# Kernel optimization log

Hardware: AMD Instinct MI355X
Metric: run time of the kernel (lower is better)

## Reference

```python
import jax, jax.numpy as jnp
import numpy as np

DIM = 512
PE_DIM = 64


def setup_inputs() -> dict:
    key = jax.random.key(0)
    k1, k2, k3, k4 = jax.random.split(key, 4)
    batch, heads, seqlen_kv = 64, 128, 4096
    return {
        "Q": jax.random.normal(k1, (batch, heads, DIM), dtype=jnp.float32),
        "Q_pe": jax.random.normal(k2, (batch, heads, PE_DIM), dtype=jnp.float32),
        "KV": jax.random.normal(k3, (batch, seqlen_kv, 1, DIM), dtype=jnp.float32),
        "K_pe": jax.random.normal(k4, (batch, seqlen_kv, 1, PE_DIM), dtype=jnp.float32),
    }


def reference(Q, Q_pe, KV, K_pe):
    # MLA decode attention with decoupled RoPE dim.
    # scores = Q @ KV^T + Q_pe @ K_pe^T, scaled by 1/sqrt(dim+pe_dim)
    # (kernel uses exp2 with log2(e)-folded scale; mathematically identical
    #  to standard softmax). Output = softmax(scores) @ KV.
    dim = Q.shape[-1]
    pe_dim = Q_pe.shape[-1]
    scale = 1.0 / np.sqrt(dim + pe_dim).astype(np.float32)
    kv = KV[:, :, 0, :]      # [b, s, dim]  (kv_head_num == 1)
    kpe = K_pe[:, :, 0, :]   # [b, s, pe_dim]
    scores = jnp.einsum('bhd,bsd->bhs', Q, kv)
    scores = scores + jnp.einsum('bhp,bsp->bhs', Q_pe, kpe)
    probs = jax.nn.softmax(scores * scale, axis=-1)  # [b, h, s]
    out = jnp.einsum('bhs,bsd->bhd', probs, kv)      # [b, h, dim]
    return out
```

## Files before the change

kernel.cpp:

```cpp
#include <hip/hip_runtime.h>

typedef _Float16 f16x8 __attribute__((ext_vector_type(8)));
typedef _Float16 f16x4 __attribute__((ext_vector_type(4)));
typedef float f32x4 __attribute__((ext_vector_type(4)));

#define B_SZ 64
#define H_SZ 128
#define S_SZ 4096
#define D_SZ 512
#define PE_SZ 64
#define NCHUNK 4
#define CHUNK 1024
#define NT 32
#define NTILES 32
#define CSCALE 0.06011229381f

#define STAGE_PITCH 516
#define KBUF_PITCH 584
#define VTB_PITCH 40
#define PB_PITCH 40
#define OB_PITCH 520

#define KBUF_OFF 66048
#define VTB_OFF 103424
#define PB_OFF 144384
#define SMEM_BYTES 154624

#define WSO_BYTES (64ull * 4 * 128 * 512 * 2)
#define WSM_OFF WSO_BYTES
#define WSL_OFF (WSO_BYTES + 64ull * 4 * 128 * 4)
#define WS_NEEDED (WSO_BYTES + 2ull * 64 * 4 * 128 * 4)

__device__ __forceinline__ void async_copy16(const float* g, float* l) {
  __builtin_amdgcn_global_load_lds(
      (const __attribute__((address_space(1))) void*)g,
      (__attribute__((address_space(3))) void*)l, 16, 0, 0);
}

__launch_bounds__(512, 2)
__global__ void mla_partial(const float* __restrict__ Q, const float* __restrict__ Qpe,
                            const float* __restrict__ KV, const float* __restrict__ Kpe,
                            _Float16* __restrict__ wsO, float* __restrict__ wsM,
                            float* __restrict__ wsL) {
  __shared__ __align__(16) char smem[SMEM_BYTES];
  float* stage   = (float*)smem;
  _Float16* kbuf = (_Float16*)(smem + KBUF_OFF);
  _Float16* vtb  = (_Float16*)(smem + VTB_OFF);
  _Float16* pb   = (_Float16*)(smem + PB_OFF);

  const int tid  = threadIdx.x;
  const int lane = tid & 63;
  const int w    = tid >> 6;
  const int quad = lane >> 4;
  const int l15  = lane & 15;

  const int b  = blockIdx.x >> 2;
  const int c  = blockIdx.x & 3;
  const int s0 = c * CHUNK;

  f16x8 qf[18];
  {
    const int h = w * 16 + l15;
    const float* qrow  = Q   + (size_t)(b * H_SZ + h) * D_SZ;
    const float* qprow = Qpe + (size_t)(b * H_SZ + h) * PE_SZ;
#pragma unroll
    for (int kk = 0; kk < 18; ++kk) {
      const float* src = (kk < 16) ? (qrow + kk * 32 + quad * 8)
                                   : (qprow + (kk - 16) * 32 + quad * 8);
      f32x4 a0 = *(const f32x4*)(src);
      f32x4 a1 = *(const f32x4*)(src + 4);
      f16x8 f;
      f[0] = (_Float16)a0[0]; f[1] = (_Float16)a0[1];
      f[2] = (_Float16)a0[2]; f[3] = (_Float16)a0[3];
      f[4] = (_Float16)a1[0]; f[5] = (_Float16)a1[1];
      f[6] = (_Float16)a1[2]; f[7] = (_Float16)a1[3];
      qf[kk] = f;
    }
  }

  f32x4 kpe_r;
  auto dma_tile = [&](int t, f32x4& kpe_out) {
    const int sg_base = b * S_SZ + s0 + t * NT;
#pragma unroll
    for (int rr = 0; rr < 4; ++rr) {
      const int row = w * 4 + rr;
      const float* gk = KV + (size_t)(sg_base + row) * D_SZ;
      float* l0 = stage + row * STAGE_PITCH;
      async_copy16(gk + lane * 4, l0 + lane * 4);
      async_copy16(gk + 256 + lane * 4, l0 + 256 + lane * 4);
    }
    kpe_out = *(const f32x4*)(Kpe + (size_t)sg_base * PE_SZ + tid * 4);
  };

  auto convert_tile = [&](f32x4 kpe_in) {
#pragma unroll
    for (int i = 0; i < 8; ++i) {
      int lin  = tid + 512 * i;
      int row  = lin >> 7;
      int col4 = lin & 127;
      f32x4 v = *(const f32x4*)(stage + row * STAGE_PITCH + col4 * 4);
      f16x4 h;
      h[0] = (_Float16)v[0]; h[1] = (_Float16)v[1];
      h[2] = (_Float16)v[2]; h[3] = (_Float16)v[3];
      *(f16x4*)(kbuf + row * KBUF_PITCH + col4 * 4) = h;
    }
    {
      int row  = tid >> 4;
      int col4 = tid & 15;
      f16x4 h;
      h[0] = (_Float16)kpe_in[0]; h[1] = (_Float16)kpe_in[1];
      h[2] = (_Float16)kpe_in[2]; h[3] = (_Float16)kpe_in[3];
      *(f16x4*)(kbuf + row * KBUF_PITCH + 512 + col4 * 4) = h;
    }
#pragma unroll
    for (int g = 0; g < 2; ++g) {
      int lin   = tid + 512 * g;
      int rg    = lin & 7;
      int cidx4 = lin >> 3;
      f32x4 v0 = *(const f32x4*)(stage + (rg * 4 + 0) * STAGE_PITCH + cidx4 * 4);
      f32x4 v1 = *(const f32x4*)(stage + (rg * 4 + 1) * STAGE_PITCH + cidx4 * 4);
      f32x4 v2 = *(const f32x4*)(stage + (rg * 4 + 2) * STAGE_PITCH + cidx4 * 4);
      f32x4 v3 = *(const f32x4*)(stage + (rg * 4 + 3) * STAGE_PITCH + cidx4 * 4);
#pragma unroll
      for (int u = 0; u < 4; ++u) {
        f16x4 h;
        h[0] = (_Float16)v0[u]; h[1] = (_Float16)v1[u];
        h[2] = (_Float16)v2[u]; h[3] = (_Float16)v3[u];
        *(f16x4*)(vtb + (cidx4 * 4 + u) * VTB_PITCH + rg * 4) = h;
      }
    }
  };

  f32x4 O[32];
#pragma unroll
  for (int i = 0; i < 32; ++i) O[i] = (f32x4){0.f, 0.f, 0.f, 0.f};
  f32x4 mr = (f32x4){-1e30f, -1e30f, -1e30f, -1e30f};
  f32x4 lr = (f32x4){0.f, 0.f, 0.f, 0.f};

  dma_tile(0, kpe_r);
  __syncthreads();
  convert_tile(kpe_r);
  __syncthreads();

  _Float16* pw = pb + w * 16 * PB_PITCH;

#pragma unroll 1
  for (int t = 0; t < NTILES; ++t) {
    f32x4 kpe_nxt;
    if (t < NTILES - 1) dma_tile(t + 1, kpe_nxt);

    f32x4 S0 = (f32x4){0.f, 0.f, 0.f, 0.f};
    f32x4 S1 = (f32x4){0.f, 0.f, 0.f, 0.f};
#pragma unroll
    for (int kk = 0; kk < 18; ++kk) {
      f16x8 b0 = *(const f16x8*)(kbuf + l15 * KBUF_PITCH + kk * 32 + quad * 8);
      f16x8 b1 = *(const f16x8*)(kbuf + (16 + l15) * KBUF_PITCH + kk * 32 + quad * 8);
      S0 = __builtin_amdgcn_mfma_f32_16x16x32_f16(qf[kk], b0, S0, 0, 0, 0);
      S1 = __builtin_amdgcn_mfma_f32_16x16x32_f16(qf[kk], b1, S1, 0, 0, 0);
    }

    f32x4 mx;
#pragma unroll
    for (int i = 0; i < 4; ++i) mx[i] = fmaxf(S0[i], S1[i]);
#pragma unroll
    for (int m = 1; m <= 8; m <<= 1) {
#pragma unroll
      for (int i = 0; i < 4; ++i) mx[i] = fmaxf(mx[i], __shfl_xor(mx[i], m, 64));
    }
    f32x4 mn, al, P0, P1, rs;
#pragma unroll
    for (int i = 0; i < 4; ++i) {
      mn[i] = fmaxf(mr[i], mx[i]);
      al[i] = exp2f((mr[i] - mn[i]) * CSCALE);
      P0[i] = exp2f((S0[i] - mn[i]) * CSCALE);
      P1[i] = exp2f((S1[i] - mn[i]) * CSCALE);
      rs[i] = P0[i] + P1[i];
    }
#pragma unroll
    for (int m = 1; m <= 8; m <<= 1) {
#pragma unroll
      for (int i = 0; i < 4; ++i) rs[i] += __shfl_xor(rs[i], m, 64);
    }
#pragma unroll
    for (int i = 0; i < 4; ++i) {
      lr[i] = lr[i] * al[i] + rs[i];
      mr[i] = mn[i];
    }

#pragma unroll
    for (int i = 0; i < 4; ++i) {
      pw[(quad * 4 + i) * PB_PITCH + l15]      = (_Float16)P0[i];
      pw[(quad * 4 + i) * PB_PITCH + 16 + l15] = (_Float16)P1[i];
    }
#pragma unroll
    for (int nt = 0; nt < 32; ++nt) O[nt] *= al;

    f16x8 pa = *(const f16x8*)(pw + l15 * PB_PITCH + quad * 8);
#pragma unroll
    for (int nt = 0; nt < 32; ++nt) {
      f16x8 bv = *(const f16x8*)(vtb + (nt * 16 + l15) * VTB_PITCH + quad * 8);
      O[nt] = __builtin_amdgcn_mfma_f32_16x16x32_f16(pa, bv, O[nt], 0, 0, 0);
    }

    __syncthreads();
    if (t < NTILES - 1) {
      convert_tile(kpe_nxt);
      __syncthreads();
    }
  }

  f32x4 inv;
#pragma unroll
  for (int i = 0; i < 4; ++i) inv[i] = 1.0f / lr[i];

  _Float16* ob = (_Float16*)smem;
#pragma unroll
  for (int nt = 0; nt < 32; ++nt) {
#pragma unroll
    for (int i = 0; i < 4; ++i) {
      ob[(w * 16 + quad * 4 + i) * OB_PITCH + nt * 16 + l15] =
          (_Float16)(O[nt][i] * inv[i]);
    }
  }
  __syncthreads();
  const size_t obase = (size_t)blockIdx.x * H_SZ * D_SZ;
#pragma unroll
  for (int j = 0; j < 16; ++j) {
    int idx = tid + 512 * j;
    int h   = idx >> 6;
    int d8  = (idx & 63) * 8;
    f16x8 v = *(const f16x8*)(ob + h * OB_PITCH + d8);
    *(f16x8*)(wsO + obase + h * D_SZ + d8) = v;
  }
  if (l15 == 0) {
    const int sbase = blockIdx.x * H_SZ + w * 16 + quad * 4;
#pragma unroll
    for (int i = 0; i < 4; ++i) {
      wsM[sbase + i] = mr[i];
      wsL[sbase + i] = lr[i];
    }
  }
}

__global__ void mla_combine(const _Float16* __restrict__ wsO, const float* __restrict__ wsM,
                            const float* __restrict__ wsL, float* __restrict__ out) {
  int tidg = blockIdx.x * 256 + threadIdx.x;
  int row  = tidg >> 6;
  int d8   = (tidg & 63) * 8;
  int b    = row >> 7;
  int h    = row & 127;

  float mv[4], lv[4];
#pragma unroll
  for (int c = 0; c < 4; ++c) {
    mv[c] = wsM[(b * 4 + c) * 128 + h];
    lv[c] = wsL[(b * 4 + c) * 128 + h];
  }
  float M = fmaxf(fmaxf(mv[0], mv[1]), fmaxf(mv[2], mv[3]));
  float wv[4], wsum = 0.f;
#pragma unroll
  for (int c = 0; c < 4; ++c) {
    wv[c] = lv[c] * exp2f((mv[c] - M) * CSCALE);
    wsum += wv[c];
  }
  float o[8] = {0.f, 0.f, 0.f, 0.f, 0.f, 0.f, 0.f, 0.f};
#pragma unroll
  for (int c = 0; c < 4; ++c) {
    f16x8 v = *(const f16x8*)(wsO + (size_t)((b * 4 + c) * 128 + h) * 512 + d8);
#pragma unroll
    for (int j = 0; j < 8; ++j) o[j] += wv[c] * (float)v[j];
  }
  float r = 1.0f / wsum;
  f32x4 r0 = (f32x4){o[0] * r, o[1] * r, o[2] * r, o[3] * r};
  f32x4 r1 = (f32x4){o[4] * r, o[5] * r, o[6] * r, o[7] * r};
  *(f32x4*)(out + (size_t)row * 512 + d8) = r0;
  *(f32x4*)(out + (size_t)row * 512 + d8 + 4) = r1;
}

extern "C" void kernel_launch(void* const* d_in, const int* in_sizes, int n_in,
                              void* d_out, int out_size, void* d_ws, size_t ws_size,
                              hipStream_t stream) {
  if (ws_size < WS_NEEDED) return;
  const float* Q   = (const float*)d_in[0];
  const float* Qpe = (const float*)d_in[1];
  const float* KV  = (const float*)d_in[2];
  const float* Kpe = (const float*)d_in[3];
  _Float16* wsO = (_Float16*)d_ws;
  float* wsM = (float*)((char*)d_ws + WSM_OFF);
  float* wsL = (float*)((char*)d_ws + WSL_OFF);

  mla_partial<<<dim3(B_SZ * NCHUNK), dim3(512), 0, stream>>>(Q, Qpe, KV, Kpe, wsO, wsM, wsL);
  mla_combine<<<dim3(2048), dim3(256), 0, stream>>>(wsO, wsM, wsL, (float*)d_out);
}
```

Measured before the change: 876.9 us.

## Transpose QK MFMA, defer softmax rescale, split PV across head-groups and D halves

The QK^T MFMA operands are swapped so each lane holds a full head row. This shrinks the row-max and row-sum reductions to two cross-quad shuffles. The running max is only raised when it grows past a threshold (lazy rescaling), and the O rescale is skipped when every alpha in the group is 1. The PV stage is re-partitioned so each wave computes 32 heads by 256 D columns, sharing its V-fragment loads across two P fragments. In exchange this adds a block barrier and LDS exchanges of P and alpha every tile, and deferred rescaling can let the probabilities reach 2^4 before fp16 conversion.

```diff
diff --git a/kernel.cpp b/kernel.cpp
--- a/kernel.cpp
+++ b/kernel.cpp
@@ -14,6 +14,7 @@
 #define NT 32
 #define NTILES 32
 #define CSCALE 0.06011229381f
+#define DEFER_LOG2 4.0f
 
 #define STAGE_PITCH 516
 #define KBUF_PITCH 584
@@ -24,7 +25,9 @@
 #define KBUF_OFF 66048
 #define VTB_OFF 103424
 #define PB_OFF 144384
-#define SMEM_BYTES 154624
+#define AL_OFF 154624
+#define LL_OFF 155136
+#define SMEM_BYTES 155648
 
 #define WSO_BYTES (64ull * 4 * 128 * 512 * 2)
 #define WSM_OFF WSO_BYTES
@@ -47,12 +50,16 @@
   _Float16* kbuf = (_Float16*)(smem + KBUF_OFF);
   _Float16* vtb  = (_Float16*)(smem + VTB_OFF);
   _Float16* pb   = (_Float16*)(smem + PB_OFF);
+  float* al_lds  = (float*)(smem + AL_OFF);
+  float* l_lds   = (float*)(smem + LL_OFF);
 
   const int tid  = threadIdx.x;
   const int lane = tid & 63;
   const int w    = tid >> 6;
   const int quad = lane >> 4;
   const int l15  = lane & 15;
+  const int hg   = w & 3;
+  const int dh   = w >> 2;
 
   const int b  = blockIdx.x >> 2;
   const int c  = blockIdx.x & 3;
@@ -134,8 +141,8 @@
   f32x4 O[32];
 #pragma unroll
   for (int i = 0; i < 32; ++i) O[i] = (f32x4){0.f, 0.f, 0.f, 0.f};
-  f32x4 mr = (f32x4){-1e30f, -1e30f, -1e30f, -1e30f};
-  f32x4 lr = (f32x4){0.f, 0.f, 0.f, 0.f};
+  float mr = -1e30f;
+  float lr = 0.f;
 
   dma_tile(0, kpe_r);
   __syncthreads();
@@ -151,55 +158,60 @@
 
     f32x4 S0 = (f32x4){0.f, 0.f, 0.f, 0.f};
     f32x4 S1 = (f32x4){0.f, 0.f, 0.f, 0.f};
+    const _Float16* kb0 = kbuf + l15 * KBUF_PITCH + quad * 8;
+    const _Float16* kb1 = kbuf + (16 + l15) * KBUF_PITCH + quad * 8;
 #pragma unroll
     for (int kk = 0; kk < 18; ++kk) {
-      f16x8 b0 = *(const f16x8*)(kbuf + l15 * KBUF_PITCH + kk * 32 + quad * 8);
-      f16x8 b1 = *(const f16x8*)(kbuf + (16 + l15) * KBUF_PITCH + kk * 32 + quad * 8);
-      S0 = __builtin_amdgcn_mfma_f32_16x16x32_f16(qf[kk], b0, S0, 0, 0, 0);
-      S1 = __builtin_amdgcn_mfma_f32_16x16x32_f16(qf[kk], b1, S1, 0, 0, 0);
-    }
-
-    f32x4 mx;
-#pragma unroll
-    for (int i = 0; i < 4; ++i) mx[i] = fmaxf(S0[i], S1[i]);
-#pragma unroll
-    for (int m = 1; m <= 8; m <<= 1) {
-#pragma unroll
-      for (int i = 0; i < 4; ++i) mx[i] = fmaxf(mx[i], __shfl_xor(mx[i], m, 64));
-    }
-    f32x4 mn, al, P0, P1, rs;
+      f16x8 b0 = *(const f16x8*)(kb0 + kk * 32);
+      f16x8 b1 = *(const f16x8*)(kb1 + kk * 32);
+      S0 = __builtin_amdgcn_mfma_f32_16x16x32_f16(b0, qf[kk], S0, 0, 0, 0);
+      S1 = __builtin_amdgcn_mfma_f32_16x16x32_f16(b1, qf[kk], S1, 0, 0, 0);
+    }
+
+    float mx = fmaxf(fmaxf(fmaxf(S0[0], S0[1]), fmaxf(S0[2], S0[3])),
+                     fmaxf(fmaxf(S1[0], S1[1]), fmaxf(S1[2], S1[3])));
+    mx = fmaxf(mx, __shfl_xor(mx, 16));
+    mx = fmaxf(mx, __shfl_xor(mx, 32));
+    const bool grow = (mx - mr) * CSCALE > DEFER_LOG2;
+    const float mn = grow ? mx : mr;
+    const float al = grow ? exp2f((mr - mn) * CSCALE) : 1.0f;
+    float p0[4], p1[4], rs = 0.f;
 #pragma unroll
     for (int i = 0; i < 4; ++i) {
-      mn[i] = fmaxf(mr[i], mx[i]);
-      al[i] = exp2f((mr[i] - mn[i]) * CSCALE);
-      P0[i] = exp2f((S0[i] - mn[i]) * CSCALE);
-      P1[i] = exp2f((S1[i] - mn[i]) * CSCALE);
-      rs[i] = P0[i] + P1[i];
-    }
-#pragma unroll
-    for (int m = 1; m <= 8; m <<= 1) {
-#pragma unroll
-      for (int i = 0; i < 4; ++i) rs[i] += __shfl_xor(rs[i], m, 64);
-    }
-#pragma unroll
-    for (int i = 0; i < 4; ++i) {
-      lr[i] = lr[i] * al[i] + rs[i];
-      mr[i] = mn[i];
-    }
-
-#pragma unroll
-    for (int i = 0; i < 4; ++i) {
-      pw[(quad * 4 + i) * PB_PITCH + l15]      = (_Float16)P0[i];
-      pw[(quad * 4 + i) * PB_PITCH + 16 + l15] = (_Float16)P1[i];
-    }
-#pragma unroll
-    for (int nt = 0; nt < 32; ++nt) O[nt] *= al;
-
-    f16x8 pa = *(const f16x8*)(pw + l15 * PB_PITCH + quad * 8);
-#pragma unroll
-    for (int nt = 0; nt < 32; ++nt) {
-      f16x8 bv = *(const f16x8*)(vtb + (nt * 16 + l15) * VTB_PITCH + quad * 8);
-      O[nt] = __builtin_amdgcn_mfma_f32_16x16x32_f16(pa, bv, O[nt], 0, 0, 0);
+      p0[i] = exp2f((S0[i] - mn) * CSCALE);
+      p1[i] = exp2f((S1[i] - mn) * CSCALE);
+      rs += p0[i] + p1[i];
+    }
+    rs += __shfl_xor(rs, 16);
+    rs += __shfl_xor(rs, 32);
+    lr = lr * al + rs;
+    mr = mn;
+
+    f16x4 h0, h1;
+#pragma unroll
+    for (int i = 0; i < 4; ++i) { h0[i] = (_Float16)p0[i]; h1[i] = (_Float16)p1[i]; }
+    *(f16x4*)(pw + l15 * PB_PITCH + quad * 4)      = h0;
+    *(f16x4*)(pw + l15 * PB_PITCH + 16 + quad * 4) = h1;
+    if (lane < 16) al_lds[w * 16 + lane] = al;
+    asm volatile("s_waitcnt lgkmcnt(0)\n\ts_barrier" ::: "memory");
+    __builtin_amdgcn_sched_barrier(0);
+
+    f32x4 av0 = *(const f32x4*)(al_lds + hg * 32 + quad * 4);
+    f32x4 av1 = *(const f32x4*)(al_lds + hg * 32 + 16 + quad * 4);
+    int stable = (av0[0] == 1.f) & (av0[1] == 1.f) & (av0[2] == 1.f) & (av0[3] == 1.f) &
+                 (av1[0] == 1.f) & (av1[1] == 1.f) & (av1[2] == 1.f) & (av1[3] == 1.f);
+    if (!__all(stable)) {
+#pragma unroll
+      for (int nt = 0; nt < 16; ++nt) { O[nt] *= av0; O[16 + nt] *= av1; }
+    }
+    f16x8 pa0 = *(const f16x8*)(pb + ((hg * 2 + 0) * 16 + l15) * PB_PITCH + quad * 8);
+    f16x8 pa1 = *(const f16x8*)(pb + ((hg * 2 + 1) * 16 + l15) * PB_PITCH + quad * 8);
+    const _Float16* vbase = vtb + (dh * 256 + l15) * VTB_PITCH + quad * 8;
+#pragma unroll
+    for (int nt = 0; nt < 16; ++nt) {
+      f16x8 bv = *(const f16x8*)(vbase + nt * 16 * VTB_PITCH);
+      O[nt]      = __builtin_amdgcn_mfma_f32_16x16x32_f16(pa0, bv, O[nt], 0, 0, 0);
+      O[16 + nt] = __builtin_amdgcn_mfma_f32_16x16x32_f16(pa1, bv, O[16 + nt], 0, 0, 0);
     }
 
     __syncthreads();
@@ -209,17 +221,28 @@
     }
   }
 
-  f32x4 inv;
-#pragma unroll
-  for (int i = 0; i < 4; ++i) inv[i] = 1.0f / lr[i];
+  if (lane < 16) {
+    l_lds[w * 16 + lane] = lr;
+    const int sbase = blockIdx.x * H_SZ + w * 16 + lane;
+    wsM[sbase] = mr;
+    wsL[sbase] = lr;
+  }
+  __syncthreads();
+  f32x4 lv0 = *(const f32x4*)(l_lds + hg * 32 + quad * 4);
+  f32x4 lv1 = *(const f32x4*)(l_lds + hg * 32 + 16 + quad * 4);
+  f32x4 iv0, iv1;
+#pragma unroll
+  for (int i = 0; i < 4; ++i) { iv0[i] = 1.0f / lv0[i]; iv1[i] = 1.0f / lv1[i]; }
 
   _Float16* ob = (_Float16*)smem;
-#pragma unroll
-  for (int nt = 0; nt < 32; ++nt) {
+  const int rb = hg * 32 + quad * 4;
+  const int cb = dh * 256 + l15;
+#pragma unroll
+  for (int nt = 0; nt < 16; ++nt) {
 #pragma unroll
     for (int i = 0; i < 4; ++i) {
-      ob[(w * 16 + quad * 4 + i) * OB_PITCH + nt * 16 + l15] =
-          (_Float16)(O[nt][i] * inv[i]);
+      ob[(rb + i) * OB_PITCH + cb + nt * 16]      = (_Float16)(O[nt][i] * iv0[i]);
+      ob[(rb + 16 + i) * OB_PITCH + cb + nt * 16] = (_Float16)(O[16 + nt][i] * iv1[i]);
     }
   }
   __syncthreads();
@@ -231,14 +254,6 @@
     int d8  = (idx & 63) * 8;
     f16x8 v = *(const f16x8*)(ob + h * OB_PITCH + d8);
     *(f16x8*)(wsO + obase + h * D_SZ + d8) = v;
-  }
-  if (l15 == 0) {
-    const int sbase = blockIdx.x * H_SZ + w * 16 + quad * 4;
-#pragma unroll
-    for (int i = 0; i < 4; ++i) {
-      wsM[sbase + i] = mr[i];
-      wsL[sbase + i] = lr[i];
-    }
   }
 }
 
```

Measured after the change: 777.0 us. 11.4% less time.
